# Performance work log

Measured on AMD Instinct MI355X. Metric: run time of the kernel, lower is better.

## Reference

```python
import jax, jax.numpy as jnp
import numpy as np

N = 50000          # nodes
E = 800000         # edges (avg degree 16)
IN = 256           # in_feats
H = 8              # num_heads
DH = 32            # out_feats // num_heads
NE = 8             # num_etypes
ALPHA = 0.2        # LeakyReLU slope


def setup_inputs() -> dict:
    key = jax.random.key(0)
    ks = jax.random.split(key, 10)
    feat = jax.random.normal(ks[0], (N, IN), dtype=jnp.float32)
    src = jax.random.randint(ks[1], (E,), 0, N, dtype=jnp.int32)
    dst = jax.random.randint(ks[2], (E,), 0, N, dtype=jnp.int32)
    etype_ids = jax.random.randint(ks[3], (E,), 0, NE, dtype=jnp.int32)
    # learned parameters (xavier-ish scale)
    W_fc = jax.random.normal(ks[4], (IN, H * DH), dtype=jnp.float32) * 0.05
    b_fc = jnp.zeros((H * DH,), dtype=jnp.float32)
    edge_emb = jax.random.normal(ks[5], (NE, H * DH), dtype=jnp.float32) * 0.05
    attn = jax.random.normal(ks[6], (1, H, 3 * DH), dtype=jnp.float32) * 0.05
    W_res = jax.random.normal(ks[7], (IN, H * DH), dtype=jnp.float32) * 0.05
    b_res = jnp.zeros((H * DH,), dtype=jnp.float32)
    return {"feat": feat, "src": src, "dst": dst, "etype_ids": etype_ids,
            "W_fc": W_fc, "b_fc": b_fc, "edge_emb": edge_emb, "attn": attn,
            "W_res": W_res, "b_res": b_res}


def reference(feat, src, dst, etype_ids, W_fc, b_fc, edge_emb, attn, W_res, b_res):
    n = feat.shape[0]
    h = (feat @ W_fc + b_fc).reshape(n, H, DH)            # [N,H,d]
    e = edge_emb[etype_ids].reshape(-1, H, DH)            # [E,H,d]
    # attn dot over concat([h_src, h_dst, e]) decomposes into 3 partial dots
    a_src = attn[0, :, :DH]
    a_dst = attn[0, :, DH:2 * DH]
    a_e = attn[0, :, 2 * DH:]
    s_src = jnp.einsum('nhd,hd->nh', h, a_src)            # [N,H]
    s_dst = jnp.einsum('nhd,hd->nh', h, a_dst)            # [N,H]
    s_e = jnp.einsum('ehd,hd->eh', e, a_e)                # [E,H]
    score = jax.nn.leaky_relu(s_src[src] + s_dst[dst] + s_e, ALPHA)  # [E,H]
    # edge softmax over incoming edges of each dst node
    mx = jax.ops.segment_max(score, dst, num_segments=n)  # [N,H]
    ex = jnp.exp(score - mx[dst])                         # [E,H]
    den = jax.ops.segment_sum(ex, dst, num_segments=n)    # [N,H]
    w = ex / den[dst]                                     # [E,H]
    # scatter-sum weighted source features to destinations
    msg = h[src] * w[:, :, None]                          # [E,H,d]
    out = jax.ops.segment_sum(msg, dst, num_segments=n).reshape(n, H * DH)
    out = out + feat @ W_res + b_res                      # residual
    return jax.nn.elu(out)
```

## Files before the change

kernel.cpp:

```cpp
#include <hip/hip_runtime.h>
#include <hip/hip_bf16.h>
#include <cstdint>

#define NN 50000
#define NEDGE 800000
#define IND 256
#define NH 8
#define DHH 32
#define NET 8
#define LALPHA 0.2f
#define OD 256
#define CD 512
#define SCAN_BLOCKS 196
#define NBG 782
#define NBH 782

typedef __attribute__((ext_vector_type(8))) short short8;
typedef __attribute__((ext_vector_type(4))) float f32x4;
typedef __attribute__((ext_vector_type(4))) float f4v;
typedef __attribute__((ext_vector_type(2))) unsigned u2v;
typedef __attribute__((ext_vector_type(4))) int i4v;

__device__ __forceinline__ unsigned short f2bf(float x) {
  union { float f; unsigned u; } v; v.f = x;
  unsigned r = v.u + 0x7FFFu + ((v.u >> 16) & 1u);
  return (unsigned short)(r >> 16);
}
__device__ __forceinline__ float bf2f(unsigned short u) {
  union { unsigned u; float f; } v; v.u = ((unsigned)u) << 16;
  return v.f;
}
__device__ __forceinline__ float u2f_lo(unsigned w) {
  union { unsigned u; float f; } v; v.u = w << 16; return v.f;
}
__device__ __forceinline__ float u2f_hi(unsigned w) {
  union { unsigned u; float f; } v; v.u = w & 0xffff0000u; return v.f;
}

__global__ __launch_bounds__(256) void k_prep(const float* __restrict__ Wfc,
                                              const float* __restrict__ Wres,
                                              unsigned short* __restrict__ Wtb,
                                              int* __restrict__ cnt,
                                              int* __restrict__ done) {
  int id = blockIdx.x * 256 + threadIdx.x;
  int k = id >> 9;
  int c = id & 511;
  float v = (c < OD) ? Wfc[k * OD + c] : Wres[k * OD + (c - OD)];
  Wtb[(size_t)c * IND + k] = f2bf(v);
  if (id < NN / 4) {
    i4v z = {0, 0, 0, 0};
    *reinterpret_cast<i4v*>(cnt + id * 4) = z;
  }
  if (id == 0) *done = 0;
}

__global__ __launch_bounds__(256, 4) void k_gemm(const float* __restrict__ Af,
                                                 const unsigned short* __restrict__ Bt,
                                                 const float* __restrict__ bfc,
                                                 const float* __restrict__ bres,
                                                 const float* __restrict__ attn,
                                                 const int* __restrict__ dst,
                                                 int* __restrict__ cnt,
                                                 int* __restrict__ rk,
                                                 unsigned short* __restrict__ Hb,
                                                 unsigned short* __restrict__ Rb,
                                                 float* __restrict__ ssrc,
                                                 float* __restrict__ sdst) {
  __shared__ unsigned short Bs[64][272];
  int tid = threadIdx.x;

  if (blockIdx.x >= NBG) {
    int e0 = ((blockIdx.x - NBG) * 256 + tid) << 2;
    if (e0 < NEDGE) {
      i4v d4 = __builtin_nontemporal_load(reinterpret_cast<const i4v*>(dst + e0));
      i4v rv;
      rv.x = atomicAdd(&cnt[d4.x], 1);
      rv.y = atomicAdd(&cnt[d4.y], 1);
      rv.z = atomicAdd(&cnt[d4.z], 1);
      rv.w = atomicAdd(&cnt[d4.w], 1);
      __builtin_nontemporal_store(rv, reinterpret_cast<i4v*>(rk + e0));
    }
    return;
  }

  int wave = tid >> 6, lane = tid & 63;
  int row0 = blockIdx.x * 64;

  int sr = tid >> 2;
  int sc = (tid & 3) * 8;

  int cl = lane & 15;
  int q = lane >> 4;
  int arow = row0 + wave * 16 + cl;
  int lrow = arow < NN ? arow : NN - 1;
  int akof = q * 8;
  short8 areg[8];
#pragma unroll
  for (int ks = 0; ks < 8; ++ks) {
    const float* p = Af + (size_t)lrow * IND + ks * 32 + akof;
    float4 f0 = *reinterpret_cast<const float4*>(p);
    float4 f1 = *reinterpret_cast<const float4*>(p + 4);
    unsigned short t8[8] = {f2bf(f0.x), f2bf(f0.y), f2bf(f0.z), f2bf(f0.w),
                            f2bf(f1.x), f2bf(f1.y), f2bf(f1.z), f2bf(f1.w)};
    areg[ks] = *reinterpret_cast<short8*>(t8);
  }

  for (int bn = 0; bn < 8; ++bn) {
    if (bn) __syncthreads();
#pragma unroll
    for (int j = 0; j < 8; ++j) {
      int k = j * 32 + sc;
      short8 bv = *reinterpret_cast<const short8*>(Bt + (size_t)(bn * 64 + sr) * IND + k);
      *reinterpret_cast<short8*>(&Bs[sr][k]) = bv;
    }
    __syncthreads();

    f32x4 acc[4];
#pragma unroll
    for (int i = 0; i < 4; ++i) acc[i] = (f32x4){0.f, 0.f, 0.f, 0.f};
#pragma unroll
    for (int ks = 0; ks < 8; ++ks) {
#pragma unroll
      for (int nf = 0; nf < 4; ++nf) {
        int colsel = (cl & 12) * 4 + (nf << 2) + (cl & 3);
        short8 b = *reinterpret_cast<const short8*>(&Bs[colsel][ks * 32 + akof]);
        acc[nf] = __builtin_amdgcn_mfma_f32_16x16x32_bf16(b, areg[ks], acc[nf], 0, 0, 0);
      }
    }

    bool isH = (bn < 4);
    int g0 = bn * 64 + q * 16;
    float s0 = 0.f, d0 = 0.f;
    unsigned short o16[16];
    if (isH) {
      int h = bn * 2 + (q >> 1);
      int dd0 = (q & 1) * 16;
#pragma unroll
      for (int nf = 0; nf < 4; ++nf) {
        f4v b4 = *reinterpret_cast<const f4v*>(bfc + g0 + nf * 4);
        f4v as4 = *reinterpret_cast<const f4v*>(attn + h * 96 + dd0 + nf * 4);
        f4v ad4 = *reinterpret_cast<const f4v*>(attn + h * 96 + 32 + dd0 + nf * 4);
#pragma unroll
        for (int r = 0; r < 4; ++r) {
          float val = acc[nf][r] + b4[r];
          o16[nf * 4 + r] = f2bf(val);
          s0 = fmaf(val, as4[r], s0);
          d0 = fmaf(val, ad4[r], d0);
        }
      }
    } else {
#pragma unroll
      for (int nf = 0; nf < 4; ++nf) {
        f4v b4 = *reinterpret_cast<const f4v*>(bres + g0 - 256 + nf * 4);
#pragma unroll
        for (int r = 0; r < 4; ++r) {
          float val = acc[nf][r] + b4[r];
          o16[nf * 4 + r] = f2bf(val);
        }
      }
    }
    if (arow < NN) {
      unsigned short* dp = isH ? (Hb + (size_t)arow * 256 + g0)
                               : (Rb + (size_t)arow * 256 + (g0 - 256));
      *reinterpret_cast<short8*>(dp) = *reinterpret_cast<short8*>(o16);
      *reinterpret_cast<short8*>(dp + 8) = *reinterpret_cast<short8*>(o16 + 8);
    }
    if (isH) {
      s0 += __shfl_xor(s0, 16);
      d0 += __shfl_xor(d0, 16);
      if (!(q & 1) && arow < NN) {
        int h = bn * 2 + (q >> 1);
        ssrc[arow * NH + h] = s0;
        sdst[arow * NH + h] = d0;
      }
    }
  }
}

__global__ __launch_bounds__(256) void k_scanA(const int* __restrict__ cnt,
                                               int* __restrict__ off,
                                               int* __restrict__ bsum,
                                               int* __restrict__ done,
                                               const float* __restrict__ ee,
                                               const float* __restrict__ attn,
                                               float* __restrict__ se,
                                               int* __restrict__ boff) {
  __shared__ int sh[256];
  __shared__ int lastFlag;
  int tid = threadIdx.x;
  int gi = blockIdx.x * 256 + tid;
  int c = (gi < NN) ? cnt[gi] : 0;
  sh[tid] = c;
  __syncthreads();
#pragma unroll
  for (int d = 1; d < 256; d <<= 1) {
    int v = (tid >= d) ? sh[tid - d] : 0;
    __syncthreads();
    sh[tid] += v;
    __syncthreads();
  }
  off[gi] = sh[tid] - c;
  if (tid == 255) {
    bsum[blockIdx.x] = sh[255];
    __threadfence();
    lastFlag = (atomicAdd(done, 1) == SCAN_BLOCKS - 1);
  }
  __syncthreads();
  if (!lastFlag) return;
  __threadfence();
  int cb = (tid < SCAN_BLOCKS)
               ? __hip_atomic_load(&bsum[tid], __ATOMIC_ACQUIRE, __HIP_MEMORY_SCOPE_AGENT)
               : 0;
  __syncthreads();
  sh[tid] = cb;
  __syncthreads();
#pragma unroll
  for (int d = 1; d < 256; d <<= 1) {
    int v = (tid >= d) ? sh[tid - d] : 0;
    __syncthreads();
    sh[tid] += v;
    __syncthreads();
  }
  boff[tid] = sh[tid] - cb;
  int h = tid >> 5, dd = tid & 31;
  float ae = attn[h * 96 + 64 + dd];
  for (int et = 0; et < NET; ++et) {
    float p = ee[et * OD + tid] * ae;
#pragma unroll
    for (int off2 = 16; off2; off2 >>= 1) p += __shfl_xor(p, off2, 32);
    if (dd == 0) se[et * NH + h] = p;
  }
}

__global__ __launch_bounds__(256) void k_scatter(const int* __restrict__ src,
                                                 const int* __restrict__ dst,
                                                 const int* __restrict__ ety,
                                                 const int* __restrict__ rk,
                                                 const int* __restrict__ off,
                                                 const int* __restrict__ boff,
                                                 int* __restrict__ csrp) {
  int t = blockIdx.x * 256 + threadIdx.x;
  int e0 = t << 2;
  if (e0 >= NEDGE) return;
  i4v s4 = __builtin_nontemporal_load(reinterpret_cast<const i4v*>(src + e0));
  i4v d4 = __builtin_nontemporal_load(reinterpret_cast<const i4v*>(dst + e0));
  i4v t4 = __builtin_nontemporal_load(reinterpret_cast<const i4v*>(ety + e0));
  i4v r4 = __builtin_nontemporal_load(reinterpret_cast<const i4v*>(rk + e0));
#pragma unroll
  for (int j = 0; j < 4; ++j) {
    int s = (j == 0) ? s4.x : (j == 1) ? s4.y : (j == 2) ? s4.z : s4.w;
    int d = (j == 0) ? d4.x : (j == 1) ? d4.y : (j == 2) ? d4.z : d4.w;
    int et = (j == 0) ? t4.x : (j == 1) ? t4.y : (j == 2) ? t4.z : t4.w;
    int r = (j == 0) ? r4.x : (j == 1) ? r4.y : (j == 2) ? r4.z : r4.w;
    csrp[off[d] + boff[d >> 8] + r] = (s << 8) | et;
  }
}

__global__ __launch_bounds__(256) void k_fuse(const unsigned short* __restrict__ Hb,
                                              const unsigned short* __restrict__ Rb,
                                              const int* __restrict__ csrp,
                                              const float* __restrict__ ssrc,
                                              const float* __restrict__ sdst,
                                              const float* __restrict__ se,
                                              const int* __restrict__ off,
                                              const int* __restrict__ boff,
                                              float* __restrict__ out) {
  __shared__ float sse[64];
  int tid = threadIdx.x;
  if (tid < 64) sse[tid] = se[tid];
  __syncthreads();
  int v = blockIdx.x * 4 + (tid >> 6);
  int lane = tid & 63;
  int g = lane >> 3;
  int hA = lane & 7;
  int lo = off[v] + boff[v >> 8];
  int hi = off[v + 1] + boff[(v + 1) >> 8];
  int n = hi - lo;
  float sd = sdst[v * NH + hA];
  unsigned lane4 = (unsigned)(lane << 2);
  float a0 = 0.f, a1 = 0.f, a2 = 0.f, a3 = 0.f, dsum = 0.f;
  for (int i = 0; i < n; i += 8) {
    int idx = i + g;
    bool ok = idx < n;
    int pk = csrp[lo + (ok ? idx : 0)];
    int uoff = pk & ~255;
    float s = ssrc[(pk >> 8) * NH + hA] + sd + sse[((pk & 255) << 3) + hA];
    s = s > 0.f ? s : LALPHA * s;
    float p = ok ? __expf(s) : 0.f;
#pragma unroll
    for (int e = 0; e < 8; ++e) {
      float pe = __shfl(p, e * 8 + g);
      unsigned ue = (unsigned)__shfl(uoff, e * 8) + lane4;
      u2v x = *reinterpret_cast<const u2v*>(Hb + ue);
      a0 = fmaf(pe, u2f_lo(x.x), a0);
      a1 = fmaf(pe, u2f_hi(x.x), a1);
      a2 = fmaf(pe, u2f_lo(x.y), a2);
      a3 = fmaf(pe, u2f_hi(x.y), a3);
      dsum += pe;
    }
  }
  unsigned oi32 = (unsigned)v * OD + lane4;
  u2v rv = __builtin_nontemporal_load(reinterpret_cast<const u2v*>(Rb + oi32));
  float inv = (dsum > 0.f) ? 1.f / dsum : 0.f;
  float o0 = fmaf(a0, inv, u2f_lo(rv.x));
  float o1 = fmaf(a1, inv, u2f_hi(rv.x));
  float o2 = fmaf(a2, inv, u2f_lo(rv.y));
  float o3 = fmaf(a3, inv, u2f_hi(rv.y));
  f4v wv;
  wv.x = o0 > 0.f ? o0 : expm1f(o0);
  wv.y = o1 > 0.f ? o1 : expm1f(o1);
  wv.z = o2 > 0.f ? o2 : expm1f(o2);
  wv.w = o3 > 0.f ? o3 : expm1f(o3);
  __builtin_nontemporal_store(wv, reinterpret_cast<f4v*>(out + (size_t)v * OD + lane4));
}

extern "C" void kernel_launch(void* const* d_in, const int* in_sizes, int n_in,
                              void* d_out, int out_size, void* d_ws, size_t ws_size,
                              hipStream_t stream) {
  const float* feat = (const float*)d_in[0];
  const int* src = (const int*)d_in[1];
  const int* dst = (const int*)d_in[2];
  const int* ety = (const int*)d_in[3];
  const float* Wfc = (const float*)d_in[4];
  const float* bfc = (const float*)d_in[5];
  const float* ee = (const float*)d_in[6];
  const float* attn = (const float*)d_in[7];
  const float* Wres = (const float*)d_in[8];
  const float* bres = (const float*)d_in[9];
  float* out = (float*)d_out;

  char* w = (char*)d_ws;
  unsigned short* Wtb   = (unsigned short*)w; w += (size_t)CD * IND * 2;
  unsigned short* Hb    = (unsigned short*)w; w += (size_t)NN * OD * 2;
  unsigned short* Rb    = (unsigned short*)w; w += (size_t)NN * OD * 2;
  float* ssrc = (float*)w; w += (size_t)NN * NH * 4;
  float* sdst = (float*)w; w += (size_t)NN * NH * 4;
  float* se   = (float*)w; w += 64 * 4;
  int* cnt    = (int*)w; w += (size_t)NN * 4;
  int* rk     = (int*)w; w += (size_t)NEDGE * 4;
  int* off    = (int*)w; w += (size_t)(SCAN_BLOCKS * 256) * 4;
  int* bsum   = (int*)w; w += 256 * 4;
  int* boff   = (int*)w; w += 256 * 4;
  int* done   = (int*)w; w += 256 * 4;
  int* csrp   = (int*)w; w += (size_t)NEDGE * 4;

  k_prep<<<(CD * IND) / 256, 256, 0, stream>>>(Wfc, Wres, Wtb, cnt, done);
  k_gemm<<<NBG + NBH, 256, 0, stream>>>(feat, Wtb, bfc, bres, attn,
                                        dst, cnt, rk, Hb, Rb, ssrc, sdst);
  k_scanA<<<SCAN_BLOCKS, 256, 0, stream>>>(cnt, off, bsum, done, ee, attn, se, boff);
  k_scatter<<<(NEDGE / 4 + 255) / 256, 256, 0, stream>>>(src, dst, ety, rk,
                                                         off, boff, csrp);
  k_fuse<<<NN / 4, 256, 0, stream>>>(Hb, Rb, csrp, ssrc, sdst, se, off, boff, out);
}
```

Baseline: 168.7 us.

## Merge scan and scatter kernels with a flag wait; widen GEMM blocks to 512 threads

The separate scatter kernel is folded into the scan kernel as extra blocks. They spin on a release/acquire flag that the last scan block sets once the block offsets are ready, which removes one kernel launch and its boundary. The GEMM kernel now runs 512-thread blocks covering 128 rows each, so each B tile loaded into LDS is reused by twice as many rows. The spin-wait assumes the scan blocks get scheduled ahead of or alongside the waiting scatter blocks; if they do not, the kernel can stall or deadlock.

```diff
diff --git a/kernel.cpp b/kernel.cpp
--- a/kernel.cpp
+++ b/kernel.cpp
@@ -12,8 +12,8 @@
 #define OD 256
 #define CD 512
 #define SCAN_BLOCKS 196
-#define NBG 782
-#define NBH 782
+#define NBG 391
+#define NBH 391
 
 typedef __attribute__((ext_vector_type(8))) short short8;
 typedef __attribute__((ext_vector_type(4))) float f32x4;
@@ -25,10 +25,6 @@
   union { float f; unsigned u; } v; v.f = x;
   unsigned r = v.u + 0x7FFFu + ((v.u >> 16) & 1u);
   return (unsigned short)(r >> 16);
-}
-__device__ __forceinline__ float bf2f(unsigned short u) {
-  union { unsigned u; float f; } v; v.u = ((unsigned)u) << 16;
-  return v.f;
 }
 __device__ __forceinline__ float u2f_lo(unsigned w) {
   union { unsigned u; float f; } v; v.u = w << 16; return v.f;
@@ -51,10 +47,10 @@
     i4v z = {0, 0, 0, 0};
     *reinterpret_cast<i4v*>(cnt + id * 4) = z;
   }
-  if (id == 0) *done = 0;
-}
-
-__global__ __launch_bounds__(256, 4) void k_gemm(const float* __restrict__ Af,
+  if (id == 0) { done[0] = 0; done[1] = 0; }
+}
+
+__global__ __launch_bounds__(512, 8) void k_gemm(const float* __restrict__ Af,
                                                  const unsigned short* __restrict__ Bt,
                                                  const float* __restrict__ bfc,
                                                  const float* __restrict__ bres,
@@ -70,7 +66,7 @@
   int tid = threadIdx.x;
 
   if (blockIdx.x >= NBG) {
-    int e0 = ((blockIdx.x - NBG) * 256 + tid) << 2;
+    int e0 = ((blockIdx.x - NBG) * 512 + tid) << 2;
     if (e0 < NEDGE) {
       i4v d4 = __builtin_nontemporal_load(reinterpret_cast<const i4v*>(dst + e0));
       i4v rv;
@@ -84,10 +80,10 @@
   }
 
   int wave = tid >> 6, lane = tid & 63;
-  int row0 = blockIdx.x * 64;
-
-  int sr = tid >> 2;
-  int sc = (tid & 3) * 8;
+  int row0 = blockIdx.x * 128;
+
+  int sr = tid >> 3;
+  int sc2 = (tid & 7) * 32;
 
   int cl = lane & 15;
   int q = lane >> 4;
@@ -108,8 +104,8 @@
   for (int bn = 0; bn < 8; ++bn) {
     if (bn) __syncthreads();
 #pragma unroll
-    for (int j = 0; j < 8; ++j) {
-      int k = j * 32 + sc;
+    for (int j = 0; j < 4; ++j) {
+      int k = sc2 + j * 8;
       short8 bv = *reinterpret_cast<const short8*>(Bt + (size_t)(bn * 64 + sr) * IND + k);
       *reinterpret_cast<short8*>(&Bs[sr][k]) = bv;
     }
@@ -177,17 +173,47 @@
   }
 }
 
-__global__ __launch_bounds__(256) void k_scanA(const int* __restrict__ cnt,
-                                               int* __restrict__ off,
-                                               int* __restrict__ bsum,
-                                               int* __restrict__ done,
-                                               const float* __restrict__ ee,
-                                               const float* __restrict__ attn,
-                                               float* __restrict__ se,
-                                               int* __restrict__ boff) {
+__global__ __launch_bounds__(256) void k_scansc(const int* __restrict__ cnt,
+                                                int* __restrict__ off,
+                                                int* __restrict__ bsum,
+                                                int* __restrict__ done,
+                                                const float* __restrict__ ee,
+                                                const float* __restrict__ attn,
+                                                float* __restrict__ se,
+                                                int* __restrict__ boff,
+                                                const int* __restrict__ src,
+                                                const int* __restrict__ dst,
+                                                const int* __restrict__ ety,
+                                                const int* __restrict__ rk,
+                                                int* __restrict__ csrp) {
+  int tid = threadIdx.x;
   __shared__ int sh[256];
   __shared__ int lastFlag;
-  int tid = threadIdx.x;
+
+  if (blockIdx.x >= SCAN_BLOCKS) {
+    if (tid == 0) {
+      while (__hip_atomic_load(done + 1, __ATOMIC_ACQUIRE, __HIP_MEMORY_SCOPE_AGENT) == 0)
+        __builtin_amdgcn_s_sleep(8);
+    }
+    __syncthreads();
+    int t = (blockIdx.x - SCAN_BLOCKS) * 256 + tid;
+    int e0 = t << 2;
+    if (e0 >= NEDGE) return;
+    i4v s4 = __builtin_nontemporal_load(reinterpret_cast<const i4v*>(src + e0));
+    i4v d4 = __builtin_nontemporal_load(reinterpret_cast<const i4v*>(dst + e0));
+    i4v t4 = __builtin_nontemporal_load(reinterpret_cast<const i4v*>(ety + e0));
+    i4v r4 = __builtin_nontemporal_load(reinterpret_cast<const i4v*>(rk + e0));
+#pragma unroll
+    for (int j = 0; j < 4; ++j) {
+      int s = (j == 0) ? s4.x : (j == 1) ? s4.y : (j == 2) ? s4.z : s4.w;
+      int d = (j == 0) ? d4.x : (j == 1) ? d4.y : (j == 2) ? d4.z : d4.w;
+      int et = (j == 0) ? t4.x : (j == 1) ? t4.y : (j == 2) ? t4.z : t4.w;
+      int r = (j == 0) ? r4.x : (j == 1) ? r4.y : (j == 2) ? r4.z : r4.w;
+      csrp[off[d] + boff[d >> 8] + r] = (s << 8) | et;
+    }
+    return;
+  }
+
   int gi = blockIdx.x * 256 + tid;
   int c = (gi < NN) ? cnt[gi] : 0;
   sh[tid] = c;
@@ -222,6 +248,11 @@
     __syncthreads();
   }
   boff[tid] = sh[tid] - cb;
+  __syncthreads();
+  if (tid == 0) {
+    __threadfence();
+    __hip_atomic_store(done + 1, 1, __ATOMIC_RELEASE, __HIP_MEMORY_SCOPE_AGENT);
+  }
   int h = tid >> 5, dd = tid & 31;
   float ae = attn[h * 96 + 64 + dd];
   for (int et = 0; et < NET; ++et) {
@@ -229,30 +260,6 @@
 #pragma unroll
     for (int off2 = 16; off2; off2 >>= 1) p += __shfl_xor(p, off2, 32);
     if (dd == 0) se[et * NH + h] = p;
-  }
-}
-
-__global__ __launch_bounds__(256) void k_scatter(const int* __restrict__ src,
-                                                 const int* __restrict__ dst,
-                                                 const int* __restrict__ ety,
-                                                 const int* __restrict__ rk,
-                                                 const int* __restrict__ off,
-                                                 const int* __restrict__ boff,
-                                                 int* __restrict__ csrp) {
-  int t = blockIdx.x * 256 + threadIdx.x;
-  int e0 = t << 2;
-  if (e0 >= NEDGE) return;
-  i4v s4 = __builtin_nontemporal_load(reinterpret_cast<const i4v*>(src + e0));
-  i4v d4 = __builtin_nontemporal_load(reinterpret_cast<const i4v*>(dst + e0));
-  i4v t4 = __builtin_nontemporal_load(reinterpret_cast<const i4v*>(ety + e0));
-  i4v r4 = __builtin_nontemporal_load(reinterpret_cast<const i4v*>(rk + e0));
-#pragma unroll
-  for (int j = 0; j < 4; ++j) {
-    int s = (j == 0) ? s4.x : (j == 1) ? s4.y : (j == 2) ? s4.z : s4.w;
-    int d = (j == 0) ? d4.x : (j == 1) ? d4.y : (j == 2) ? d4.z : d4.w;
-    int et = (j == 0) ? t4.x : (j == 1) ? t4.y : (j == 2) ? t4.z : t4.w;
-    int r = (j == 0) ? r4.x : (j == 1) ? r4.y : (j == 2) ? r4.z : r4.w;
-    csrp[off[d] + boff[d >> 8] + r] = (s << 8) | et;
   }
 }
 
@@ -345,10 +352,9 @@
   int* csrp   = (int*)w; w += (size_t)NEDGE * 4;
 
   k_prep<<<(CD * IND) / 256, 256, 0, stream>>>(Wfc, Wres, Wtb, cnt, done);
-  k_gemm<<<NBG + NBH, 256, 0, stream>>>(feat, Wtb, bfc, bres, attn,
+  k_gemm<<<NBG + NBH, 512, 0, stream>>>(feat, Wtb, bfc, bres, attn,
                                         dst, cnt, rk, Hb, Rb, ssrc, sdst);
-  k_scanA<<<SCAN_BLOCKS, 256, 0, stream>>>(cnt, off, bsum, done, ee, attn, se, boff);
-  k_scatter<<<(NEDGE / 4 + 255) / 256, 256, 0, stream>>>(src, dst, ety, rk,
-                                                         off, boff, csrp);
+  k_scansc<<<SCAN_BLOCKS + 782, 256, 0, stream>>>(cnt, off, bsum, done, ee, attn,
+                                                  se, boff, src, dst, ety, rk, csrp);
   k_fuse<<<NN / 4, 256, 0, stream>>>(Hb, Rb, csrp, ssrc, sdst, se, off, boff, out);
 }
```

Measured after the change: 287.2 us. 1.7x slower.
